# Kernel tuning notes

Measured on AMD Instinct MI355X. Metric: run time of the kernel, lower is better.

The kernel has to match this reference:

```python
import jax, jax.numpy as jnp
import numpy as np

B, S, H, UNITS = 32, 2048, 1024, 1024


def setup_inputs() -> dict:
    key = jax.random.key(0)
    ks = jax.random.split(key, 5)
    scale = 1.0 / np.sqrt(H)
    return {
        "query": jax.random.normal(ks[0], (B, H), dtype=jnp.float32),
        "values": jax.random.normal(ks[1], (B, S, H), dtype=jnp.float32),
        "W1": jax.random.normal(ks[2], (H, UNITS), dtype=jnp.float32) * scale,
        "b1": jnp.zeros((UNITS,), dtype=jnp.float32),
        "W2": jax.random.normal(ks[3], (H, UNITS), dtype=jnp.float32) * scale,
        "b2": jnp.zeros((UNITS,), dtype=jnp.float32),
        "V": jax.random.normal(ks[4], (UNITS, 1), dtype=jnp.float32) * (1.0 / np.sqrt(UNITS)),
        "bV": jnp.zeros((1,), dtype=jnp.float32),
    }


def reference(query, values, W1, b1, W2, b2, V, bV):
    # W1(values): [B,S,U]; W2(query): [B,1,U] broadcast over S
    proj_v = jnp.einsum("bsh,hu->bsu", values, W1) + b1
    proj_q = (query @ W2 + b2)[:, None, :]
    score = jnp.tanh(proj_v + proj_q) @ V + bV          # [B,S,1]
    attention_weights = jax.nn.softmax(score, axis=1)   # softmax over seq
    context_vector = jnp.sum(attention_weights * values, axis=1)  # [B,H]
    return (attention_weights, context_vector)
```

## Files before the change

### kernel.cpp

```cpp
#include <hip/hip_runtime.h>
#include <hip/hip_bf16.h>
#include <stdint.h>

#define B_ 32
#define S_ 2048
#define H_ 1024
#define U_ 1024

typedef __attribute__((ext_vector_type(8))) short short8;
typedef __attribute__((ext_vector_type(4))) float f32x4;

#define AS1 __attribute__((address_space(1)))
#define AS3 __attribute__((address_space(3)))
#define FENCE __builtin_amdgcn_sched_barrier(0)

__device__ __forceinline__ unsigned short f2bf(float f) {
  unsigned int u = __float_as_uint(f);
  u += 0x7fffu + ((u >> 16) & 1u);
  return (unsigned short)(u >> 16);
}
__device__ __forceinline__ float bf2f(unsigned short s) {
  return __uint_as_float(((unsigned int)s) << 16);
}

__global__ void k_cvt(const float* __restrict__ v, unsigned short* __restrict__ o) {
  const size_t n = (size_t)B_ * S_ * H_;
  const size_t stride = (size_t)gridDim.x * blockDim.x * 8;
  for (size_t i = ((size_t)blockIdx.x * blockDim.x + threadIdx.x) * 8; i < n; i += stride) {
    float4 a = *(const float4*)(v + i), b = *(const float4*)(v + i + 4);
    short8 w;
    w[0]=f2bf(a.x); w[1]=f2bf(a.y); w[2]=f2bf(a.z); w[3]=f2bf(a.w);
    w[4]=f2bf(b.x); w[5]=f2bf(b.y); w[6]=f2bf(b.z); w[7]=f2bf(b.w);
    *(short8*)(o + i) = w;
  }
}

__global__ void k_transpose_w1(const float* __restrict__ W1, unsigned short* __restrict__ W1T) {
  __shared__ float tile[64][65];
  const int tx = threadIdx.x, ty = threadIdx.y;
  const int u0 = blockIdx.x * 64, h0 = blockIdx.y * 64;
#pragma unroll
  for (int i = 0; i < 16; ++i) {
    int hl = ty + i * 4;
    tile[hl][tx] = W1[(size_t)(h0 + hl) * U_ + (u0 + tx)];
  }
  __syncthreads();
#pragma unroll
  for (int i = 0; i < 16; ++i) {
    int ul = ty + i * 4;
    W1T[(size_t)(u0 + ul) * H_ + (h0 + tx)] = f2bf(tile[tx][ul]);
  }
}

__global__ void k_b1q_part(const float* __restrict__ query, const float* __restrict__ W2,
                           float* __restrict__ qpart) {
  __shared__ float q_sh[32 * 128];
  const int u = blockIdx.x * 256 + threadIdx.x;
  const int hs = blockIdx.y;
  for (int i = threadIdx.x; i < 4096; i += 256) {
    const int b = i >> 7, h = i & 127;
    q_sh[i] = query[b * H_ + hs * 128 + h];
  }
  __syncthreads();
  float acc[32];
#pragma unroll
  for (int b = 0; b < 32; ++b) acc[b] = 0.f;
  for (int h = 0; h < 128; ++h) {
    const float w = W2[(size_t)(hs * 128 + h) * U_ + u];
#pragma unroll
    for (int b = 0; b < 32; ++b) acc[b] += q_sh[b * 128 + h] * w;
  }
#pragma unroll
  for (int b = 0; b < 32; ++b) qpart[((size_t)hs * 32 + b) * U_ + u] = acc[b];
}

__global__ void k_b1q_comb(const float* __restrict__ qpart, const float* __restrict__ b1,
                           const float* __restrict__ b2, float* __restrict__ b1q) {
  const int u = blockIdx.x * 256 + threadIdx.x;
  const int b = blockIdx.y;
  float s = b1[u] + b2[u];
#pragma unroll
  for (int hs = 0; hs < 8; ++hs) s += qpart[((size_t)hs * 32 + b) * U_ + u];
  b1q[b * U_ + u] = s;
}

#define BM 128
#define BN 256
#define BK 32
#define NSTEP 32

__global__ __launch_bounds__(512, 4)
void k_fused_score(const unsigned short* __restrict__ vbf,
                   const unsigned short* __restrict__ W1T,
                   const float* __restrict__ b1q, const float* __restrict__ V,
                   float* __restrict__ score_part) {
  __shared__ __align__(16) unsigned char smem[73728];
  unsigned short* As = (unsigned short*)smem;
  unsigned short* Bs = (unsigned short*)(smem + 24576);
  float* scorebuf = (float*)smem;

  const int tid = threadIdx.x;
  const int g = blockIdx.x;
  const int seq = (g & 7) * 256 + (g >> 3);
  const int bn = seq & 3;
  const int bm = seq >> 2;

  const int lane = tid & 63, wid = tid >> 6;
  const int wm = wid >> 2, wn = wid & 3;
  const int u0 = bn * BN;

  const int arow = tid >> 2;
  const int alc = (tid & 3) ^ ((arow >> 1) & 3);
  const unsigned short* pa  = vbf + (size_t)(bm * BM + arow) * H_ + alc * 8;
  const unsigned short* pb0 = W1T + (size_t)(u0 + arow) * H_ + alc * 8;
  const unsigned short* pb1 = pb0 + (size_t)128 * H_;

  const int l15 = lane & 15, l16 = lane >> 4;
  const int fsq = ((l16 ^ ((lane >> 1) & 3)) << 3);
  const int pA = (wm * 64 + l15) * 32 + fsq;
  const int pB = (wn * 64 + l15) * 32 + fsq;

  f32x4 acc[4][4];
#pragma unroll
  for (int mf = 0; mf < 4; ++mf)
#pragma unroll
    for (int nf = 0; nf < 4; ++nf) acc[mf][nf] = (f32x4){0.f, 0.f, 0.f, 0.f};

#define STAGE_K(SLOT, KOFF) { \
    __builtin_amdgcn_global_load_lds((const AS1 void*)(pa + (KOFF)),  \
        (AS3 void*)&As[(SLOT) * 4096 + tid * 8], 16, 0, 0); \
    __builtin_amdgcn_global_load_lds((const AS1 void*)(pb0 + (KOFF)), \
        (AS3 void*)&Bs[(SLOT) * 8192 + tid * 8], 16, 0, 0); \
    __builtin_amdgcn_global_load_lds((const AS1 void*)(pb1 + (KOFF)), \
        (AS3 void*)&Bs[(SLOT) * 8192 + 4096 + tid * 8], 16, 0, 0); }

#define COMPUTE(SC) { \
    short8 af[4], bv[4]; \
    _Pragma("unroll") \
    for (int mf = 0; mf < 4; ++mf) \
      af[mf] = *(const short8*)&As[(SC) * 4096 + pA + mf * 512]; \
    _Pragma("unroll") \
    for (int nf = 0; nf < 4; ++nf) \
      bv[nf] = *(const short8*)&Bs[(SC) * 8192 + pB + nf * 512]; \
    _Pragma("unroll") \
    for (int nf = 0; nf < 4; ++nf) \
      _Pragma("unroll") \
      for (int mf = 0; mf < 4; ++mf) \
        acc[mf][nf] = __builtin_amdgcn_mfma_f32_16x16x32_bf16(af[mf], bv[nf], acc[mf][nf], 0, 0, 0); }

#define SUBSTEP(SC, SN, KOFF) { \
    STAGE_K(SN, KOFF); \
    FENCE; \
    COMPUTE(SC); \
    FENCE; \
    asm volatile("s_waitcnt vmcnt(3)" ::: "memory"); \
    FENCE; \
    __builtin_amdgcn_s_barrier(); }

  STAGE_K(0, 0);
  STAGE_K(1, 32);
  asm volatile("s_waitcnt vmcnt(3)" ::: "memory");
  FENCE;
  __builtin_amdgcn_s_barrier();

  for (int it = 0; it < 10; ++it) {
    SUBSTEP(0, 2, 64);
    SUBSTEP(1, 0, 96);
    SUBSTEP(2, 1, 128);
    pa += 96; pb0 += 96; pb1 += 96;
  }
  {
    COMPUTE(0);
    FENCE;
    asm volatile("s_waitcnt vmcnt(0)" ::: "memory");
    FENCE;
    __builtin_amdgcn_s_barrier();
    COMPUTE(1);
  }

  __syncthreads();
  const int b_blk = bm >> 4;
  float bqv[4], vvv[4];
#pragma unroll
  for (int nf = 0; nf < 4; ++nf) {
    const int ug = u0 + wn * 64 + nf * 16 + l15;
    bqv[nf] = b1q[b_blk * U_ + ug];
    vvv[nf] = V[ug];
  }
  float rp[4][4];
#pragma unroll
  for (int mf = 0; mf < 4; ++mf)
#pragma unroll
    for (int j = 0; j < 4; ++j) rp[mf][j] = 0.f;
#pragma unroll
  for (int nf = 0; nf < 4; ++nf)
#pragma unroll
    for (int mf = 0; mf < 4; ++mf) {
      const f32x4 c = acc[mf][nf];
#pragma unroll
      for (int j = 0; j < 4; ++j) {
        const float x = c[j] + bqv[nf];
        const float e = __expf(2.f * x);
        const float tt = 1.f - 2.f / (e + 1.f);
        rp[mf][j] += tt * vvv[nf];
      }
    }
#pragma unroll
  for (int mf = 0; mf < 4; ++mf)
#pragma unroll
    for (int j = 0; j < 4; ++j) {
      float v = rp[mf][j];
      v += __shfl_xor(v, 1);
      v += __shfl_xor(v, 2);
      v += __shfl_xor(v, 4);
      v += __shfl_xor(v, 8);
      rp[mf][j] = v;
    }
  if (l15 == 0) {
#pragma unroll
    for (int mf = 0; mf < 4; ++mf)
#pragma unroll
      for (int j = 0; j < 4; ++j)
        scorebuf[(wm * 64 + mf * 16 + l16 * 4 + j) * 4 + wn] = rp[mf][j];
  }
  __syncthreads();
  if (tid < BM) {
    const float s = scorebuf[tid * 4 + 0] + scorebuf[tid * 4 + 1] +
                    scorebuf[tid * 4 + 2] + scorebuf[tid * 4 + 3];
    score_part[(size_t)bn * (B_ * S_) + bm * BM + tid] = s;
  }
}

__global__ void k_softmax(const float* __restrict__ sp, float* __restrict__ aw) {
  __shared__ float red[8];
  const int b = blockIdx.x, tid = threadIdx.x;
  const int BS = B_ * S_;
  float x[8];
  float m = -1e30f;
#pragma unroll
  for (int i = 0; i < 8; ++i) {
    const int s = b * S_ + tid + i * 256;
    x[i] = sp[s] + sp[BS + s] + sp[2 * BS + s] + sp[3 * BS + s];
    m = fmaxf(m, x[i]);
  }
#pragma unroll
  for (int off = 32; off; off >>= 1) m = fmaxf(m, __shfl_xor(m, off));
  if ((tid & 63) == 0) red[tid >> 6] = m;
  __syncthreads();
  m = fmaxf(fmaxf(red[0], red[1]), fmaxf(red[2], red[3]));
  float e[8];
  float sum = 0.f;
#pragma unroll
  for (int i = 0; i < 8; ++i) { e[i] = __expf(x[i] - m); sum += e[i]; }
#pragma unroll
  for (int off = 32; off; off >>= 1) sum += __shfl_xor(sum, off);
  __syncthreads();
  if ((tid & 63) == 0) red[4 + (tid >> 6)] = sum;
  __syncthreads();
  sum = red[4] + red[5] + red[6] + red[7];
  const float inv = 1.f / sum;
#pragma unroll
  for (int i = 0; i < 8; ++i) aw[b * S_ + tid + i * 256] = e[i] * inv;
}

__global__ void k_ctx_partial(const unsigned short* __restrict__ vbf, const float* __restrict__ aw,
                              float* __restrict__ part) {
  __shared__ float a_s[128];
  const int b = blockIdx.y, sc = blockIdx.x, tid = threadIdx.x;
  if (tid < 128) a_s[tid] = aw[b * S_ + sc * 128 + tid];
  __syncthreads();
  const unsigned short* vp = vbf + (size_t)(b * S_ + sc * 128) * H_ + tid * 4;
  float4 acc = {0.f, 0.f, 0.f, 0.f};
#pragma unroll 4
  for (int i = 0; i < 128; ++i) {
    const ushort4 v = *(const ushort4*)(vp + (size_t)i * H_);
    const float a = a_s[i];
    acc.x += a * bf2f(v.x); acc.y += a * bf2f(v.y);
    acc.z += a * bf2f(v.z); acc.w += a * bf2f(v.w);
  }
  ((float4*)part)[(size_t)(b * 16 + sc) * (H_ / 4) + tid] = acc;
}

__global__ void k_ctx_combine(const float* __restrict__ part, float* __restrict__ ctx) {
  const int b = blockIdx.x, tid = threadIdx.x;
  float4 s = {0.f, 0.f, 0.f, 0.f};
#pragma unroll
  for (int c = 0; c < 16; ++c) {
    const float4 v = ((const float4*)part)[(size_t)(b * 16 + c) * (H_ / 4) + tid];
    s.x += v.x; s.y += v.y; s.z += v.z; s.w += v.w;
  }
  ((float4*)ctx)[b * (H_ / 4) + tid] = s;
}

extern "C" void kernel_launch(void* const* d_in, const int* in_sizes, int n_in,
                              void* d_out, int out_size, void* d_ws, size_t ws_size,
                              hipStream_t stream) {
  const float* query  = (const float*)d_in[0];
  const float* values = (const float*)d_in[1];
  const float* W1     = (const float*)d_in[2];
  const float* b1     = (const float*)d_in[3];
  const float* W2     = (const float*)d_in[4];
  const float* b2     = (const float*)d_in[5];
  const float* V      = (const float*)d_in[6];

  char* ws = (char*)d_ws;
  unsigned short* W1T = (unsigned short*)ws;
  float* b1q   = (float*)(ws + 2u * 1024u * 1024u);
  float* spart = (float*)(ws + 2u * 1024u * 1024u + 128u * 1024u);
  float* cpart = (float*)(ws + 3u * 1024u * 1024u + 128u * 1024u);
  float* qpart = (float*)(ws + 5u * 1024u * 1024u + 128u * 1024u);
  unsigned short* vbf = (unsigned short*)(ws + 8u * 1024u * 1024u);

  float* aw  = (float*)d_out;
  float* ctx = aw + B_ * S_;

  k_transpose_w1<<<dim3(16, 16), dim3(64, 4), 0, stream>>>(W1, W1T);
  k_b1q_part<<<dim3(4, 8), dim3(256), 0, stream>>>(query, W2, qpart);
  k_b1q_comb<<<dim3(4, 32), dim3(256), 0, stream>>>(qpart, b1, b2, b1q);
  k_cvt<<<dim3(2048), dim3(256), 0, stream>>>(values, vbf);
  k_fused_score<<<dim3(2048), dim3(512), 0, stream>>>(vbf, W1T, b1q, V, spart);
  k_softmax<<<dim3(32), dim3(256), 0, stream>>>(spart, aw);
  k_ctx_partial<<<dim3(16, 32), dim3(256), 0, stream>>>(vbf, aw, cpart);
  k_ctx_combine<<<dim3(32), dim3(256), 0, stream>>>(cpart, ctx);
}
```

Measured before the change: 306.0 us.

## Enlarge score GEMM tile to 256x256 with BK=64 phased half-tile pipeline

```diff
diff --git a/kernel.cpp b/kernel.cpp
--- a/kernel.cpp
+++ b/kernel.cpp
@@ -13,6 +13,8 @@
 #define AS1 __attribute__((address_space(1)))
 #define AS3 __attribute__((address_space(3)))
 #define FENCE __builtin_amdgcn_sched_barrier(0)
+#define LGKM0 asm volatile("s_waitcnt lgkmcnt(0)" ::: "memory")
+#define VMC4  asm volatile("s_waitcnt vmcnt(4)" ::: "memory")
 
 __device__ __forceinline__ unsigned short f2bf(float f) {
   unsigned int u = __float_as_uint(f);
@@ -84,102 +86,122 @@
   b1q[b * U_ + u] = s;
 }
 
-#define BM 128
-#define BN 256
-#define BK 32
-#define NSTEP 32
-
-__global__ __launch_bounds__(512, 4)
+#define BMT 256
+#define BNT 256
+#define NKT 16
+
+__global__ __launch_bounds__(512, 2)
 void k_fused_score(const unsigned short* __restrict__ vbf,
                    const unsigned short* __restrict__ W1T,
                    const float* __restrict__ b1q, const float* __restrict__ V,
                    float* __restrict__ score_part) {
-  __shared__ __align__(16) unsigned char smem[73728];
-  unsigned short* As = (unsigned short*)smem;
-  unsigned short* Bs = (unsigned short*)(smem + 24576);
+  __shared__ __align__(16) unsigned char smem[131072];
+  unsigned short* Ash = (unsigned short*)smem;
+  unsigned short* Bsh = (unsigned short*)(smem + 65536);
   float* scorebuf = (float*)smem;
 
   const int tid = threadIdx.x;
   const int g = blockIdx.x;
-  const int seq = (g & 7) * 256 + (g >> 3);
+  const int seq = (g & 7) * 128 + (g >> 3);
   const int bn = seq & 3;
   const int bm = seq >> 2;
 
   const int lane = tid & 63, wid = tid >> 6;
   const int wm = wid >> 2, wn = wid & 3;
-  const int u0 = bn * BN;
-
-  const int arow = tid >> 2;
-  const int alc = (tid & 3) ^ ((arow >> 1) & 3);
-  const unsigned short* pa  = vbf + (size_t)(bm * BM + arow) * H_ + alc * 8;
-  const unsigned short* pb0 = W1T + (size_t)(u0 + arow) * H_ + alc * 8;
-  const unsigned short* pb1 = pb0 + (size_t)128 * H_;
-
-  const int l15 = lane & 15, l16 = lane >> 4;
-  const int fsq = ((l16 ^ ((lane >> 1) & 3)) << 3);
-  const int pA = (wm * 64 + l15) * 32 + fsq;
-  const int pB = (wn * 64 + l15) * 32 + fsq;
-
-  f32x4 acc[4][4];
-#pragma unroll
-  for (int mf = 0; mf < 4; ++mf)
+  const int u0 = bn * BNT;
+
+  const int r0 = tid >> 3;
+  const int c0 = tid & 7;
+  const int lc = c0 ^ (r0 & 7);
+  const unsigned short* paS = vbf + (size_t)(bm * BMT + r0) * H_ + lc * 8;
+  const unsigned short* pbS = W1T + (size_t)(u0 + r0) * H_ + lc * 8;
+  const int dOff = tid * 16;
+
+  const int l15 = lane & 15, l16 = lane >> 4, l7 = lane & 7;
+  const int pAk0 = (wm * 128 + l15) * 64 + ((0 + l16) ^ l7) * 8;
+  const int pAk1 = (wm * 128 + l15) * 64 + ((4 + l16) ^ l7) * 8;
+  const int pBk0 = (wn * 64 + l15) * 64 + ((0 + l16) ^ l7) * 8;
+  const int pBk1 = (wn * 64 + l15) * 64 + ((4 + l16) ^ l7) * 8;
+
+  f32x4 acc[8][4];
+#pragma unroll
+  for (int mf = 0; mf < 8; ++mf)
 #pragma unroll
     for (int nf = 0; nf < 4; ++nf) acc[mf][nf] = (f32x4){0.f, 0.f, 0.f, 0.f};
 
-#define STAGE_K(SLOT, KOFF) { \
-    __builtin_amdgcn_global_load_lds((const AS1 void*)(pa + (KOFF)),  \
-        (AS3 void*)&As[(SLOT) * 4096 + tid * 8], 16, 0, 0); \
-    __builtin_amdgcn_global_load_lds((const AS1 void*)(pb0 + (KOFF)), \
-        (AS3 void*)&Bs[(SLOT) * 8192 + tid * 8], 16, 0, 0); \
-    __builtin_amdgcn_global_load_lds((const AS1 void*)(pb1 + (KOFF)), \
-        (AS3 void*)&Bs[(SLOT) * 8192 + 4096 + tid * 8], 16, 0, 0); }
-
-#define COMPUTE(SC) { \
-    short8 af[4], bv[4]; \
+  short8 af0, af1, af2, af3;
+  short8 bv[4][2];
+
+#define STAGEH(OP, D, H, TK) { \
+    const unsigned short* s0_ = ((OP) ? pbS : paS) + (size_t)(H) * 128 * H_ + (TK); \
+    const unsigned short* s1_ = s0_ + (size_t)64 * H_; \
+    unsigned char* dst_ = smem + (OP) * 65536 + (D) * 32768 + (H) * 16384 + dOff; \
+    __builtin_amdgcn_global_load_lds((const AS1 void*)s0_, (AS3 void*)dst_, 16, 0, 0); \
+    __builtin_amdgcn_global_load_lds((const AS1 void*)s1_, (AS3 void*)(dst_ + 8192), 16, 0, 0); }
+
+#define READ_AF(D, Q) { \
+    af0 = *(const short8*)&Ash[(D) * 16384 + (2*(Q)+0) * 1024 + pAk0]; \
+    af1 = *(const short8*)&Ash[(D) * 16384 + (2*(Q)+0) * 1024 + pAk1]; \
+    af2 = *(const short8*)&Ash[(D) * 16384 + (2*(Q)+1) * 1024 + pAk0]; \
+    af3 = *(const short8*)&Ash[(D) * 16384 + (2*(Q)+1) * 1024 + pAk1]; }
+
+#define READ_BV(D) { \
     _Pragma("unroll") \
-    for (int mf = 0; mf < 4; ++mf) \
-      af[mf] = *(const short8*)&As[(SC) * 4096 + pA + mf * 512]; \
+    for (int nf_ = 0; nf_ < 4; ++nf_) { \
+      bv[nf_][0] = *(const short8*)&Bsh[(D) * 16384 + nf_ * 1024 + pBk0]; \
+      bv[nf_][1] = *(const short8*)&Bsh[(D) * 16384 + nf_ * 1024 + pBk1]; } }
+
+#define MFMA16(Q) { \
+    __builtin_amdgcn_s_setprio(1); \
     _Pragma("unroll") \
-    for (int nf = 0; nf < 4; ++nf) \
-      bv[nf] = *(const short8*)&Bs[(SC) * 8192 + pB + nf * 512]; \
-    _Pragma("unroll") \
-    for (int nf = 0; nf < 4; ++nf) \
-      _Pragma("unroll") \
-      for (int mf = 0; mf < 4; ++mf) \
-        acc[mf][nf] = __builtin_amdgcn_mfma_f32_16x16x32_bf16(af[mf], bv[nf], acc[mf][nf], 0, 0, 0); }
-
-#define SUBSTEP(SC, SN, KOFF) { \
-    STAGE_K(SN, KOFF); \
+    for (int nf_ = 0; nf_ < 4; ++nf_) { \
+      acc[2*(Q)+0][nf_] = __builtin_amdgcn_mfma_f32_16x16x32_bf16(af0, bv[nf_][0], acc[2*(Q)+0][nf_], 0, 0, 0); \
+      acc[2*(Q)+1][nf_] = __builtin_amdgcn_mfma_f32_16x16x32_bf16(af2, bv[nf_][0], acc[2*(Q)+1][nf_], 0, 0, 0); \
+      acc[2*(Q)+0][nf_] = __builtin_amdgcn_mfma_f32_16x16x32_bf16(af1, bv[nf_][1], acc[2*(Q)+0][nf_], 0, 0, 0); \
+      acc[2*(Q)+1][nf_] = __builtin_amdgcn_mfma_f32_16x16x32_bf16(af3, bv[nf_][1], acc[2*(Q)+1][nf_], 0, 0, 0); \
+    } \
+    __builtin_amdgcn_s_setprio(0); }
+
+#define PHASE(DC, Q, RDBV, OPS, DS, HS, TKS, DOVMC) { \
+    if (RDBV) READ_BV(DC); \
+    READ_AF(DC, Q); \
+    STAGEH(OPS, DS, HS, TKS); \
     FENCE; \
-    COMPUTE(SC); \
+    __builtin_amdgcn_s_barrier(); \
+    LGKM0; \
     FENCE; \
-    asm volatile("s_waitcnt vmcnt(3)" ::: "memory"); \
+    MFMA16(Q); \
     FENCE; \
+    if (DOVMC) { VMC4; FENCE; } \
     __builtin_amdgcn_s_barrier(); }
 
-  STAGE_K(0, 0);
-  STAGE_K(1, 32);
-  asm volatile("s_waitcnt vmcnt(3)" ::: "memory");
+  STAGEH(0, 0, 0, 0);  STAGEH(0, 0, 1, 0);
+  STAGEH(1, 0, 0, 0);  STAGEH(1, 0, 1, 0);
+  STAGEH(1, 1, 0, 64); STAGEH(1, 1, 1, 64);
+  VMC4;
   FENCE;
   __builtin_amdgcn_s_barrier();
 
-  for (int it = 0; it < 10; ++it) {
-    SUBSTEP(0, 2, 64);
-    SUBSTEP(1, 0, 96);
-    SUBSTEP(2, 1, 128);
-    pa += 96; pb0 += 96; pb1 += 96;
-  }
-  {
-    COMPUTE(0);
-    FENCE;
-    asm volatile("s_waitcnt vmcnt(0)" ::: "memory");
-    FENCE;
-    __builtin_amdgcn_s_barrier();
-    COMPUTE(1);
-  }
-
-  __syncthreads();
-  const int b_blk = bm >> 4;
+  for (int i = 0; i < 8; ++i) {
+    const int t = 2 * i;
+    const int kA1 = (t + 1) * 64;
+    const int kB2 = ((t + 2 < NKT) ? t + 2 : NKT - 1) * 64;
+    const int kA2 = kB2;
+    const int kB3 = ((t + 3 < NKT) ? t + 3 : NKT - 1) * 64;
+    PHASE(0, 0, 1, 0, 1, 0, kA1, 0);
+    PHASE(0, 1, 0, 0, 1, 1, kA1, 0);
+    PHASE(0, 2, 0, 1, 0, 0, kB2, 0);
+    PHASE(0, 3, 0, 1, 0, 1, kB2, 1);
+    PHASE(1, 0, 1, 0, 0, 0, kA2, 0);
+    PHASE(1, 1, 0, 0, 0, 1, kA2, 0);
+    PHASE(1, 2, 0, 1, 1, 0, kB3, 0);
+    PHASE(1, 3, 0, 1, 1, 1, kB3, 1);
+  }
+  asm volatile("s_waitcnt vmcnt(0)" ::: "memory");
+  FENCE;
+  __builtin_amdgcn_s_barrier();
+
+  const int b_blk = bm >> 3;
   float bqv[4], vvv[4];
 #pragma unroll
   for (int nf = 0; nf < 4; ++nf) {
@@ -187,15 +209,15 @@
     bqv[nf] = b1q[b_blk * U_ + ug];
     vvv[nf] = V[ug];
   }
-  float rp[4][4];
-#pragma unroll
-  for (int mf = 0; mf < 4; ++mf)
+  float rp[8][4];
+#pragma unroll
+  for (int mf = 0; mf < 8; ++mf)
 #pragma unroll
     for (int j = 0; j < 4; ++j) rp[mf][j] = 0.f;
 #pragma unroll
   for (int nf = 0; nf < 4; ++nf)
 #pragma unroll
-    for (int mf = 0; mf < 4; ++mf) {
+    for (int mf = 0; mf < 8; ++mf) {
       const f32x4 c = acc[mf][nf];
 #pragma unroll
       for (int j = 0; j < 4; ++j) {
@@ -206,7 +228,7 @@
       }
     }
 #pragma unroll
-  for (int mf = 0; mf < 4; ++mf)
+  for (int mf = 0; mf < 8; ++mf)
 #pragma unroll
     for (int j = 0; j < 4; ++j) {
       float v = rp[mf][j];
@@ -218,16 +240,16 @@
     }
   if (l15 == 0) {
 #pragma unroll
-    for (int mf = 0; mf < 4; ++mf)
+    for (int mf = 0; mf < 8; ++mf)
 #pragma unroll
       for (int j = 0; j < 4; ++j)
-        scorebuf[(wm * 64 + mf * 16 + l16 * 4 + j) * 4 + wn] = rp[mf][j];
-  }
-  __syncthreads();
-  if (tid < BM) {
+        scorebuf[(wm * 128 + mf * 16 + l16 * 4 + j) * 4 + wn] = rp[mf][j];
+  }
+  __syncthreads();
+  if (tid < BMT) {
     const float s = scorebuf[tid * 4 + 0] + scorebuf[tid * 4 + 1] +
                     scorebuf[tid * 4 + 2] + scorebuf[tid * 4 + 3];
-    score_part[(size_t)bn * (B_ * S_) + bm * BM + tid] = s;
+    score_part[(size_t)bn * (B_ * S_) + bm * BMT + tid] = s;
   }
 }
 
@@ -318,7 +340,7 @@
   k_b1q_part<<<dim3(4, 8), dim3(256), 0, stream>>>(query, W2, qpart);
   k_b1q_comb<<<dim3(4, 32), dim3(256), 0, stream>>>(qpart, b1, b2, b1q);
   k_cvt<<<dim3(2048), dim3(256), 0, stream>>>(values, vbf);
-  k_fused_score<<<dim3(2048), dim3(512), 0, stream>>>(vbf, W1T, b1q, V, spart);
+  k_fused_score<<<dim3(1024), dim3(512), 0, stream>>>(vbf, W1T, b1q, V, spart);
   k_softmax<<<dim3(32), dim3(256), 0, stream>>>(spart, aw);
   k_ctx_partial<<<dim3(16, 32), dim3(256), 0, stream>>>(vbf, aw, cpart);
   k_ctx_combine<<<dim3(32), dim3(256), 0, stream>>>(cpart, ctx);
```

Result: faster. 292.5 us (-4.4%).
